# Performance work log

Hardware: AMD Instinct MI355X
Metric: run time of the kernel (lower is better)

## Reference

```python
import jax, jax.numpy as jnp
import numpy as np

B, S, D, H = 1024, 64, 1024, 32
HD = D // H  # 32


def make_rpe_map():
    # one-hot map from 225 relative offsets (15x15) to 64x64 (q,k) board pairs
    out = np.zeros((225, 64 * 64), dtype=np.float32)
    for i in range(8):
        for j in range(8):
            for k in range(8):
                for m in range(8):
                    out[15 * (i - k + 7) + (j - m + 7), 64 * (i * 8 + j) + k * 8 + m] = 1
    return out


RPE_MAP = jnp.asarray(make_rpe_map())  # [225, 4096]


def setup_inputs() -> dict:
    key = jax.random.key(0)
    ks = jax.random.split(key, 11)
    s = 0.02
    return {
        "x": jax.random.normal(ks[0], (B, S, D), jnp.float32),
        "q_w": jax.random.normal(ks[1], (D, D), jnp.float32) * s,
        "q_b": jax.random.normal(ks[2], (D,), jnp.float32) * s,
        "k_w": jax.random.normal(ks[3], (D, D), jnp.float32) * s,
        "k_b": jax.random.normal(ks[4], (D,), jnp.float32) * s,
        "v_w": jax.random.normal(ks[5], (D, D), jnp.float32) * s,
        "v_b": jax.random.normal(ks[6], (D,), jnp.float32) * s,
        "out_w": jax.random.normal(ks[7], (D, D), jnp.float32) * s,
        "out_b": jax.random.normal(ks[8], (D,), jnp.float32) * s,
        "rpe_q_w": jax.random.normal(ks[9], (HD * H, 225), jnp.float32) * s,
        "rpe_k_w": jax.random.normal(ks[10], (HD * H, 225), jnp.float32) * s,
    }


def reference(x, q_w, q_b, k_w, k_b, v_w, v_b, out_w, out_b, rpe_q_w, rpe_k_w):
    b, s, _ = x.shape

    def proj(w, bias):
        # torch Linear: y = x @ w.T + b ; then [B,S,H,HD] -> [B,H,S,HD]
        return (x @ w.T + bias).reshape(b, s, H, HD).transpose(0, 2, 1, 3)

    q = proj(q_w, q_b)
    k = proj(k_w, k_b)
    v = proj(v_w, v_b)

    scores = jnp.einsum('bhqd,bhkd->bhqk', q, k)
    bias_q = (rpe_q_w @ RPE_MAP).reshape(HD, H, 64, 64)  # [d,h,q,k]
    scores = scores + jnp.einsum('bhqd,dhqk->bhqk', q, bias_q)
    bias_k = (rpe_k_w @ RPE_MAP).reshape(HD, H, 64, 64)
    scores = scores + jnp.einsum('bhkd,dhqk->bhqk', k, bias_k)
    scores = scores / jnp.sqrt(jnp.asarray(HD, scores.dtype))

    attn = jax.nn.softmax(scores, axis=-1)
    out = jnp.einsum('bhqk,bhkd->bhqd', attn, v)
    out = out.transpose(0, 2, 1, 3).reshape(b, s, D)
    return out @ out_w.T + out_b
```

## Files before the change

### kernel.cpp

```cpp
#include <hip/hip_runtime.h>
#include <hip/hip_bf16.h>

#define AS1 __attribute__((address_space(1)))
#define AS3 __attribute__((address_space(3)))

typedef __attribute__((ext_vector_type(4))) float f32x4;
typedef __attribute__((ext_vector_type(8))) short b16x8;
typedef __attribute__((ext_vector_type(8))) unsigned short u16x8;
typedef unsigned short u16;

static __device__ __forceinline__ u16 f2b(float f) {
  return __builtin_bit_cast(u16, __float2bfloat16(f));
}
static __device__ __forceinline__ float b2f(u16 u) {
  unsigned v = ((unsigned)u) << 16;
  return __builtin_bit_cast(float, v);
}
static __device__ __forceinline__ void gl2lds16(const u16* g, u16* l) {
  __builtin_amdgcn_global_load_lds((const AS1 void*)g, (AS3 void*)l, 16, 0, 0);
}

__global__ void k_cvt(const float* __restrict__ s, u16* __restrict__ d, long n) {
  long i = ((long)blockIdx.x * 256 + threadIdx.x) * 8;
  if (i >= n) return;
  float4 a = *(const float4*)(s + i);
  float4 b = *(const float4*)(s + i + 4);
  u16x8 o;
  o[0] = f2b(a.x); o[1] = f2b(a.y); o[2] = f2b(a.z); o[3] = f2b(a.w);
  o[4] = f2b(b.x); o[5] = f2b(b.y); o[6] = f2b(b.z); o[7] = f2b(b.w);
  *(u16x8*)(d + i) = o;
}

__global__ void k_rpe(const float* __restrict__ rq, const float* __restrict__ rk,
                      u16* __restrict__ oq, u16* __restrict__ ok) {
  int h = blockIdx.y;
  int r = blockIdx.x * 8 + (threadIdx.x >> 5);
  int d = threadIdx.x & 31;
  const float* s = blockIdx.z ? rk : rq;
  u16* o = blockIdx.z ? ok : oq;
  float v = (r < 225) ? s[(d * 32 + h) * 225 + r] : 0.f;
  o[(h * 240 + r) * 32 + d] = f2b(v);
}

template <int MODE>
__global__ __launch_bounds__(512) void k_gemm(
    const u16* __restrict__ A, const u16* __restrict__ Bw,
    const float* __restrict__ b0, const float* __restrict__ b1, const float* __restrict__ b2,
    u16* __restrict__ oq, float* __restrict__ of) {
  __shared__ alignas(16) u16 lds[4][16384];
  const int tid = threadIdx.x;
  const int l = tid & 63, w = tid >> 6;
  const int lo = l & 15, hi = l >> 4;
  const int wr = w >> 2, wc = w & 3;

  const int nbx = gridDim.x;
  const int nb = nbx * gridDim.y;
  const int bid = blockIdx.y * nbx + blockIdx.x;
  const int ord = (bid & 7) * (nb >> 3) + (bid >> 3);
  const int tn = (ord % nbx) * 256, tm = (ord / nbx) * 256;

  const int sl = (tid & 7) ^ ((tid >> 3) & 7);
  const int srow = 2 * (tid >> 3) + (sl >> 2);
  const int scol = (sl & 3) * 8;
  const u16* gA = A + (size_t)(tm + srow) * 1024 + scol;
  const u16* gB = Bw + (size_t)(tn + srow) * 1024 + scol;
  u16* dst = &lds[0][0] + tid * 8;

  const int p7 = (lo >> 1) & 7;
  const int slr = ((lo & 1) * 4 + hi) ^ p7;
  const int aoff = wr * 4096 + (lo >> 1) * 64 + slr * 8;
  const int boff = 8192 + wc * 2048 + (lo >> 1) * 64 + slr * 8;

  f32x4 acc[8][4];
#pragma unroll
  for (int i = 0; i < 8; ++i)
#pragma unroll
    for (int j = 0; j < 4; ++j) acc[i][j] = (f32x4){0.f, 0.f, 0.f, 0.f};

#define STG(kt) { const int kc = (kt) * 32; u16* d = dst + ((kt) & 3) * 16384; \
    gl2lds16(gA + kc, d);           gl2lds16(gA + 131072 + kc, d + 4096); \
    gl2lds16(gB + kc, d + 8192);    gl2lds16(gB + 131072 + kc, d + 12288); }

  STG(0) STG(1) STG(2)
  asm volatile("s_waitcnt vmcnt(8)" ::: "memory");
  __builtin_amdgcn_s_barrier();
  asm volatile("" ::: "memory");

#pragma unroll 4
  for (int kt = 0; kt < 32; ++kt) {
    if (kt < 29) STG(kt + 3);
    const u16* bufA = &lds[kt & 3][0] + aoff;
    const u16* bufB = &lds[kt & 3][0] + boff;
    b16x8 af[8], bf[4];
#pragma unroll
    for (int i = 0; i < 8; ++i) af[i] = *(const b16x8*)(bufA + i * 512);
#pragma unroll
    for (int j = 0; j < 4; ++j) bf[j] = *(const b16x8*)(bufB + j * 512);
    __builtin_amdgcn_s_setprio(1);
#pragma unroll
    for (int i = 0; i < 8; ++i)
#pragma unroll
      for (int j = 0; j < 4; ++j)
        acc[i][j] = __builtin_amdgcn_mfma_f32_16x16x32_bf16(af[i], bf[j], acc[i][j], 0, 0, 0);
    __builtin_amdgcn_s_setprio(0);
    if (kt < 29)       asm volatile("s_waitcnt vmcnt(8)" ::: "memory");
    else if (kt == 29) asm volatile("s_waitcnt vmcnt(4)" ::: "memory");
    else if (kt == 30) asm volatile("s_waitcnt vmcnt(0)" ::: "memory");
    if (kt < 31) {
      __builtin_amdgcn_s_barrier();
      asm volatile("" ::: "memory");
    }
  }
#undef STG

  if (MODE == 0) {
    const size_t G = 67108864;
    const int g = tn >> 10;
    const float* bias = (g == 0) ? b0 : (g == 1) ? b1 : b2;
    const int nn0 = (tn & 1023) + wc * 64;
#pragma unroll
    for (int j = 0; j < 4; ++j) {
      const int nn = nn0 + j * 16 + lo;
      const float bv = bias[nn];
      const int h = nn >> 5, hd = nn & 31;
      if (g < 2) {
#pragma unroll
        for (int i = 0; i < 8; ++i) {
          const int m0 = tm + wr * 128 + i * 16 + hi * 4;
          const int b = m0 >> 6, s0 = m0 & 63;
          const size_t base = (size_t)g * G + ((size_t)(b * 32 + h) * 64 + s0) * 32 + hd;
#pragma unroll
          for (int r = 0; r < 4; ++r) oq[base + (size_t)r * 32] = f2b(acc[i][j][r] + bv);
        }
      } else {
#pragma unroll
        for (int i = 0; i < 8; ++i) {
          const int m0 = tm + wr * 128 + i * 16 + hi * 4;
          const int b = m0 >> 6, s0 = m0 & 63;
          ushort4 pk;
          pk.x = f2b(acc[i][j][0] + bv);
          pk.y = f2b(acc[i][j][1] + bv);
          pk.z = f2b(acc[i][j][2] + bv);
          pk.w = f2b(acc[i][j][3] + bv);
          *(ushort4*)(oq + 2 * G + ((size_t)(b * 32 + h) * 32 + hd) * 64 + s0) = pk;
        }
      }
    }
  } else {
#pragma unroll
    for (int j = 0; j < 4; ++j) {
      const int n = tn + wc * 64 + j * 16 + lo;
      const float bv = b0[n];
#pragma unroll
      for (int i = 0; i < 8; ++i) {
        const int m0 = tm + wr * 128 + i * 16 + hi * 4;
#pragma unroll
        for (int r = 0; r < 4; ++r) of[(size_t)(m0 + r) * 1024 + n] = acc[i][j][r] + bv;
      }
    }
  }
}

__global__ __launch_bounds__(256) void k_attn(
    const u16* __restrict__ qkv, const u16* __restrict__ rq,
    const u16* __restrict__ rk, u16* __restrict__ att) {
  __shared__ alignas(16) u16 buf[64 * 244];
  __shared__ alignas(16) u16 pl[64 * 72];
  const int l = threadIdx.x & 63, w = threadIdx.x >> 6;
  const int lo = l & 15, hi = l >> 4;
  const int b = blockIdx.x, h = blockIdx.y;
  const size_t G = 67108864;
  const u16* qp = qkv + (size_t)(b * 32 + h) * 2048;
  const u16* kp = qkv + G + (size_t)(b * 32 + h) * 2048;
  const u16* vp = qkv + 2 * G + (size_t)(b * 32 + h) * 2048;

  b16x8 qf = *(const b16x8*)(qp + (w * 16 + lo) * 32 + hi * 8);

  f32x4 s0[4];
#pragma unroll
  for (int kt = 0; kt < 4; ++kt) {
    b16x8 kf = *(const b16x8*)(kp + (kt * 16 + lo) * 32 + hi * 8);
    f32x4 z = (f32x4){0.f, 0.f, 0.f, 0.f};
    s0[kt] = __builtin_amdgcn_mfma_f32_16x16x32_bf16(qf, kf, z, 0, 0, 0);
  }

  const u16* rqh = rq + (size_t)h * 7680;
#pragma unroll
  for (int nt = 0; nt < 15; ++nt) {
    b16x8 rf = *(const b16x8*)(rqh + (nt * 16 + lo) * 32 + hi * 8);
    f32x4 z = (f32x4){0.f, 0.f, 0.f, 0.f};
    f32x4 c = __builtin_amdgcn_mfma_f32_16x16x32_bf16(qf, rf, z, 0, 0, 0);
#pragma unroll
    for (int r = 0; r < 4; ++r) buf[(w * 16 + hi * 4 + r) * 244 + nt * 16 + lo] = f2b(c[r]);
  }
#pragma unroll
  for (int kt = 0; kt < 4; ++kt)
#pragma unroll
    for (int r = 0; r < 4; ++r) {
      int q = w * 16 + hi * 4 + r, k = kt * 16 + lo;
      int rel = 15 * ((q >> 3) - (k >> 3) + 7) + (q & 7) - (k & 7) + 7;
      s0[kt][r] += b2f(buf[q * 244 + rel]);
    }

  b16x8 kfa = *(const b16x8*)(kp + (w * 16 + lo) * 32 + hi * 8);
  const u16* rkh = rk + (size_t)h * 7680;
#pragma unroll
  for (int nt = 0; nt < 15; ++nt) {
    b16x8 rf = *(const b16x8*)(rkh + (nt * 16 + lo) * 32 + hi * 8);
    f32x4 z = (f32x4){0.f, 0.f, 0.f, 0.f};
    f32x4 c = __builtin_amdgcn_mfma_f32_16x16x32_bf16(kfa, rf, z, 0, 0, 0);
#pragma unroll
    for (int r = 0; r < 4; ++r) buf[(w * 16 + hi * 4 + r) * 244 + nt * 16 + lo] = f2b(c[r]);
  }
  __syncthreads();
#pragma unroll
  for (int kt = 0; kt < 4; ++kt)
#pragma unroll
    for (int r = 0; r < 4; ++r) {
      int q = w * 16 + hi * 4 + r, k = kt * 16 + lo;
      int rel = 15 * ((q >> 3) - (k >> 3) + 7) + (q & 7) - (k & 7) + 7;
      s0[kt][r] += b2f(buf[k * 244 + rel]);
    }

  const float sc = 0.17677669529663689f;
#pragma unroll
  for (int kt = 0; kt < 4; ++kt) s0[kt] *= sc;
  float p[4][4], rsum[4];
#pragma unroll
  for (int r = 0; r < 4; ++r) {
    float m = s0[0][r];
    m = fmaxf(m, s0[1][r]); m = fmaxf(m, s0[2][r]); m = fmaxf(m, s0[3][r]);
    m = fmaxf(m, __shfl_xor(m, 1));
    m = fmaxf(m, __shfl_xor(m, 2));
    m = fmaxf(m, __shfl_xor(m, 4));
    m = fmaxf(m, __shfl_xor(m, 8));
    float sum = 0.f;
#pragma unroll
    for (int kt = 0; kt < 4; ++kt) {
      float e = __expf(s0[kt][r] - m);
      p[kt][r] = e;
      sum += e;
    }
    sum += __shfl_xor(sum, 1);
    sum += __shfl_xor(sum, 2);
    sum += __shfl_xor(sum, 4);
    sum += __shfl_xor(sum, 8);
    rsum[r] = 1.f / sum;
  }

#pragma unroll
  for (int kt = 0; kt < 4; ++kt)
#pragma unroll
    for (int r = 0; r < 4; ++r) pl[(w * 16 + hi * 4 + r) * 72 + kt * 16 + lo] = f2b(p[kt][r]);

  f32x4 o0 = (f32x4){0.f, 0.f, 0.f, 0.f}, o1 = (f32x4){0.f, 0.f, 0.f, 0.f};
#pragma unroll
  for (int ks = 0; ks < 2; ++ks) {
    b16x8 pa = *(const b16x8*)(pl + (w * 16 + lo) * 72 + ks * 32 + hi * 8);
    b16x8 v0 = *(const b16x8*)(vp + lo * 64 + ks * 32 + hi * 8);
    b16x8 v1 = *(const b16x8*)(vp + (16 + lo) * 64 + ks * 32 + hi * 8);
    o0 = __builtin_amdgcn_mfma_f32_16x16x32_bf16(pa, v0, o0, 0, 0, 0);
    o1 = __builtin_amdgcn_mfma_f32_16x16x32_bf16(pa, v1, o1, 0, 0, 0);
  }

#pragma unroll
  for (int r = 0; r < 4; ++r) {
    int q = w * 16 + hi * 4 + r;
    size_t base = (size_t)(b * 64 + q) * 1024 + h * 32;
    att[base + lo] = f2b(o0[r] * rsum[r]);
    att[base + 16 + lo] = f2b(o1[r] * rsum[r]);
  }
}

extern "C" void kernel_launch(void* const* d_in, const int* in_sizes, int n_in,
                              void* d_out, int out_size, void* d_ws, size_t ws_size,
                              hipStream_t stream) {
  const float* x   = (const float*)d_in[0];
  const float* qw  = (const float*)d_in[1];
  const float* qb  = (const float*)d_in[2];
  const float* kw  = (const float*)d_in[3];
  const float* kb  = (const float*)d_in[4];
  const float* vw  = (const float*)d_in[5];
  const float* vb  = (const float*)d_in[6];
  const float* ow  = (const float*)d_in[7];
  const float* ob  = (const float*)d_in[8];
  const float* rqw = (const float*)d_in[9];
  const float* rkw = (const float*)d_in[10];

  if (ws_size < 680460288ULL) return;
  char* p = (char*)d_ws;
  u16* ws_x   = (u16*)p; p += (size_t)65536 * 1024 * 2;
  u16* ws_w   = (u16*)p; p += (size_t)3 * 1024 * 1024 * 2;
  u16* ws_wo  = (u16*)p; p += (size_t)1024 * 1024 * 2;
  u16* ws_rq  = (u16*)p; p += (size_t)32 * 240 * 32 * 2;
  u16* ws_rk  = (u16*)p; p += (size_t)32 * 240 * 32 * 2;
  u16* ws_qkv = (u16*)p; p += (size_t)3 * 67108864 * 2;
  u16* ws_att = (u16*)p; p += (size_t)65536 * 1024 * 2;

  k_cvt<<<32768, 256, 0, stream>>>(x, ws_x, 67108864L);
  k_cvt<<<512, 256, 0, stream>>>(qw, ws_w, 1048576L);
  k_cvt<<<512, 256, 0, stream>>>(kw, ws_w + 1048576, 1048576L);
  k_cvt<<<512, 256, 0, stream>>>(vw, ws_w + 2097152, 1048576L);
  k_cvt<<<512, 256, 0, stream>>>(ow, ws_wo, 1048576L);
  k_rpe<<<dim3(30, 32, 2), 256, 0, stream>>>(rqw, rkw, ws_rq, ws_rk);

  k_gemm<0><<<dim3(12, 256), 512, 0, stream>>>(ws_x, ws_w, qb, kb, vb, ws_qkv, nullptr);
  k_attn<<<dim3(1024, 32), 256, 0, stream>>>(ws_qkv, ws_rq, ws_rk, ws_att);
  k_gemm<1><<<dim3(4, 256), 512, 0, stream>>>(ws_att, ws_wo, ob, nullptr, nullptr, nullptr,
                                              (float*)d_out);
}
```

Baseline: 1.034 ms.

## Double-buffer GEMM LDS fragments and repack attention RPE scratch layout

The GEMM main loop is software-pipelined with two register fragment sets, so the LDS reads for the next k-tile are issued before the MFMAs of the current tile and LDS latency overlaps with compute. In the attention kernel, the RPE bias scratch is repacked so each lane stores its four results with one 8-byte write, and the same LDS region is reused for the softmax probabilities after an added barrier. V fragments are also loaded from global memory up front to hide their latency. The changes raise register pressure and add one more block-wide synchronisation.

New measurement: 1.020 ms. About the same (-1.4%).

```diff
diff --git a/kernel.cpp b/kernel.cpp
--- a/kernel.cpp
+++ b/kernel.cpp
@@ -77,41 +77,50 @@
 #pragma unroll
     for (int j = 0; j < 4; ++j) acc[i][j] = (f32x4){0.f, 0.f, 0.f, 0.f};
 
-#define STG(kt) { const int kc = (kt) * 32; u16* d = dst + ((kt) & 3) * 16384; \
+#define STG(t) { const int kc = (t) * 32; u16* d = dst + ((t) & 3) * 16384; \
     gl2lds16(gA + kc, d);           gl2lds16(gA + 131072 + kc, d + 4096); \
     gl2lds16(gB + kc, d + 8192);    gl2lds16(gB + 131072 + kc, d + 12288); }
+#define RDF(fa, fb, bi) { const u16* _b = &lds[0][0] + (bi) * 16384; \
+    _Pragma("unroll") for (int _i = 0; _i < 8; ++_i) fa[_i] = *(const b16x8*)(_b + aoff + _i * 512); \
+    _Pragma("unroll") for (int _j = 0; _j < 4; ++_j) fb[_j] = *(const b16x8*)(_b + boff + _j * 512); }
+#define MMS(fa, fb) { __builtin_amdgcn_s_setprio(1); \
+    _Pragma("unroll") for (int _i = 0; _i < 8; ++_i) \
+    _Pragma("unroll") for (int _j = 0; _j < 4; ++_j) \
+      acc[_i][_j] = __builtin_amdgcn_mfma_f32_16x16x32_bf16(fa[_i], fb[_j], acc[_i][_j], 0, 0, 0); \
+    __builtin_amdgcn_s_setprio(0); }
+#define WB(n) { asm volatile("s_waitcnt vmcnt(" #n ")" ::: "memory"); \
+    __builtin_amdgcn_s_barrier(); asm volatile("" ::: "memory"); }
+
+  b16x8 fa0[8], fb0[4], fa1[8], fb1[4];
 
   STG(0) STG(1) STG(2)
-  asm volatile("s_waitcnt vmcnt(8)" ::: "memory");
-  __builtin_amdgcn_s_barrier();
-  asm volatile("" ::: "memory");
-
-#pragma unroll 4
-  for (int kt = 0; kt < 32; ++kt) {
-    if (kt < 29) STG(kt + 3);
-    const u16* bufA = &lds[kt & 3][0] + aoff;
-    const u16* bufB = &lds[kt & 3][0] + boff;
-    b16x8 af[8], bf[4];
-#pragma unroll
-    for (int i = 0; i < 8; ++i) af[i] = *(const b16x8*)(bufA + i * 512);
-#pragma unroll
-    for (int j = 0; j < 4; ++j) bf[j] = *(const b16x8*)(bufB + j * 512);
-    __builtin_amdgcn_s_setprio(1);
-#pragma unroll
-    for (int i = 0; i < 8; ++i)
-#pragma unroll
-      for (int j = 0; j < 4; ++j)
-        acc[i][j] = __builtin_amdgcn_mfma_f32_16x16x32_bf16(af[i], bf[j], acc[i][j], 0, 0, 0);
-    __builtin_amdgcn_s_setprio(0);
-    if (kt < 29)       asm volatile("s_waitcnt vmcnt(8)" ::: "memory");
-    else if (kt == 29) asm volatile("s_waitcnt vmcnt(4)" ::: "memory");
-    else if (kt == 30) asm volatile("s_waitcnt vmcnt(0)" ::: "memory");
-    if (kt < 31) {
-      __builtin_amdgcn_s_barrier();
-      asm volatile("" ::: "memory");
-    }
-  }
+  WB(4)
+  RDF(fa0, fb0, 0)
+
+  for (int kt = 0; kt < 28; kt += 2) {
+    STG(kt + 3)
+    RDF(fa1, fb1, (kt + 1) & 3)
+    MMS(fa0, fb0)
+    WB(4)
+    STG(kt + 4)
+    RDF(fa0, fb0, (kt + 2) & 3)
+    MMS(fa1, fb1)
+    WB(4)
+  }
+  STG(31)
+  RDF(fa1, fb1, 1)
+  MMS(fa0, fb0)
+  WB(4)
+  RDF(fa0, fb0, 2)
+  MMS(fa1, fb1)
+  WB(0)
+  RDF(fa1, fb1, 3)
+  MMS(fa0, fb0)
+  MMS(fa1, fb1)
 #undef STG
+#undef RDF
+#undef MMS
+#undef WB
 
   if (MODE == 0) {
     const size_t G = 67108864;
@@ -164,8 +173,8 @@
 __global__ __launch_bounds__(256) void k_attn(
     const u16* __restrict__ qkv, const u16* __restrict__ rq,
     const u16* __restrict__ rk, u16* __restrict__ att) {
-  __shared__ alignas(16) u16 buf[64 * 244];
-  __shared__ alignas(16) u16 pl[64 * 72];
+  __shared__ alignas(16) u16 board[16 * 240 * 4];
+  u16* pl = board;
   const int l = threadIdx.x & 63, w = threadIdx.x >> 6;
   const int lo = l & 15, hi = l >> 4;
   const int b = blockIdx.x, h = blockIdx.y;
@@ -175,6 +184,10 @@
   const u16* vp = qkv + 2 * G + (size_t)(b * 32 + h) * 2048;
 
   b16x8 qf = *(const b16x8*)(qp + (w * 16 + lo) * 32 + hi * 8);
+  b16x8 v00 = *(const b16x8*)(vp + lo * 64 + hi * 8);
+  b16x8 v01 = *(const b16x8*)(vp + lo * 64 + 32 + hi * 8);
+  b16x8 v10 = *(const b16x8*)(vp + (16 + lo) * 64 + hi * 8);
+  b16x8 v11 = *(const b16x8*)(vp + (16 + lo) * 64 + 32 + hi * 8);
 
   f32x4 s0[4];
 #pragma unroll
@@ -190,8 +203,9 @@
     b16x8 rf = *(const b16x8*)(rqh + (nt * 16 + lo) * 32 + hi * 8);
     f32x4 z = (f32x4){0.f, 0.f, 0.f, 0.f};
     f32x4 c = __builtin_amdgcn_mfma_f32_16x16x32_bf16(qf, rf, z, 0, 0, 0);
-#pragma unroll
-    for (int r = 0; r < 4; ++r) buf[(w * 16 + hi * 4 + r) * 244 + nt * 16 + lo] = f2b(c[r]);
+    ushort4 pk;
+    pk.x = f2b(c[0]); pk.y = f2b(c[1]); pk.z = f2b(c[2]); pk.w = f2b(c[3]);
+    *(ushort4*)(board + (((w * 4 + hi) * 240 + nt * 16 + lo) << 2)) = pk;
   }
 #pragma unroll
   for (int kt = 0; kt < 4; ++kt)
@@ -199,7 +213,7 @@
     for (int r = 0; r < 4; ++r) {
       int q = w * 16 + hi * 4 + r, k = kt * 16 + lo;
       int rel = 15 * ((q >> 3) - (k >> 3) + 7) + (q & 7) - (k & 7) + 7;
-      s0[kt][r] += b2f(buf[q * 244 + rel]);
+      s0[kt][r] += b2f(board[((w * 4 + hi) * 240 + rel) * 4 + r]);
     }
 
   b16x8 kfa = *(const b16x8*)(kp + (w * 16 + lo) * 32 + hi * 8);
@@ -209,8 +223,9 @@
     b16x8 rf = *(const b16x8*)(rkh + (nt * 16 + lo) * 32 + hi * 8);
     f32x4 z = (f32x4){0.f, 0.f, 0.f, 0.f};
     f32x4 c = __builtin_amdgcn_mfma_f32_16x16x32_bf16(kfa, rf, z, 0, 0, 0);
-#pragma unroll
-    for (int r = 0; r < 4; ++r) buf[(w * 16 + hi * 4 + r) * 244 + nt * 16 + lo] = f2b(c[r]);
+    ushort4 pk;
+    pk.x = f2b(c[0]); pk.y = f2b(c[1]); pk.z = f2b(c[2]); pk.w = f2b(c[3]);
+    *(ushort4*)(board + (((w * 4 + hi) * 240 + nt * 16 + lo) << 2)) = pk;
   }
   __syncthreads();
 #pragma unroll
@@ -219,7 +234,7 @@
     for (int r = 0; r < 4; ++r) {
       int q = w * 16 + hi * 4 + r, k = kt * 16 + lo;
       int rel = 15 * ((q >> 3) - (k >> 3) + 7) + (q & 7) - (k & 7) + 7;
-      s0[kt][r] += b2f(buf[k * 244 + rel]);
+      s0[kt][r] += b2f(board[((k >> 2) * 240 + rel) * 4 + (k & 3)]);
     }
 
   const float sc = 0.17677669529663689f;
@@ -248,19 +263,21 @@
     rsum[r] = 1.f / sum;
   }
 
+  __syncthreads();
+
 #pragma unroll
   for (int kt = 0; kt < 4; ++kt)
 #pragma unroll
     for (int r = 0; r < 4; ++r) pl[(w * 16 + hi * 4 + r) * 72 + kt * 16 + lo] = f2b(p[kt][r]);
 
   f32x4 o0 = (f32x4){0.f, 0.f, 0.f, 0.f}, o1 = (f32x4){0.f, 0.f, 0.f, 0.f};
-#pragma unroll
-  for (int ks = 0; ks < 2; ++ks) {
-    b16x8 pa = *(const b16x8*)(pl + (w * 16 + lo) * 72 + ks * 32 + hi * 8);
-    b16x8 v0 = *(const b16x8*)(vp + lo * 64 + ks * 32 + hi * 8);
-    b16x8 v1 = *(const b16x8*)(vp + (16 + lo) * 64 + ks * 32 + hi * 8);
-    o0 = __builtin_amdgcn_mfma_f32_16x16x32_bf16(pa, v0, o0, 0, 0, 0);
-    o1 = __builtin_amdgcn_mfma_f32_16x16x32_bf16(pa, v1, o1, 0, 0, 0);
+  {
+    b16x8 pa0 = *(const b16x8*)(pl + (w * 16 + lo) * 72 + hi * 8);
+    b16x8 pa1 = *(const b16x8*)(pl + (w * 16 + lo) * 72 + 32 + hi * 8);
+    o0 = __builtin_amdgcn_mfma_f32_16x16x32_bf16(pa0, v00, o0, 0, 0, 0);
+    o1 = __builtin_amdgcn_mfma_f32_16x16x32_bf16(pa0, v10, o1, 0, 0, 0);
+    o0 = __builtin_amdgcn_mfma_f32_16x16x32_bf16(pa1, v01, o0, 0, 0, 0);
+    o1 = __builtin_amdgcn_mfma_f32_16x16x32_bf16(pa1, v11, o1, 0, 0, 0);
   }
 
 #pragma unroll
```
